# Performance work log

Hardware: AMD Instinct MI355X
Metric: run time of the kernel (lower is better)

## Reference

```python
import jax, jax.numpy as jnp
import numpy as np
from jax import lax

CONF_THR = 0.1
IOU_THR = 0.45
B, C, IMG = 4, 20, 416.0
SIZES = {"p3": 8112, "p4": 2028, "p5": 507}


def setup_inputs() -> dict:
    key = jax.random.key(0)
    ks = jax.random.split(key, 4 * len(SIZES))
    d = {}
    i = 0
    for name, n in SIZES.items():
        # valid xyxy boxes: random centers in image, widths/heights in [4, 104]
        cxy = jax.random.uniform(ks[i], (B, n, 2), jnp.float32) * IMG
        wh = jax.random.uniform(ks[i + 1], (B, n, 2), jnp.float32) * 100.0 + 4.0
        d[f"{name}_boxes"] = jnp.concatenate([cxy - wh / 2, cxy + wh / 2], axis=-1)
        d[f"{name}_conf"] = jax.random.uniform(ks[i + 2], (B, n, 1), jnp.float32)
        d[f"{name}_cls"] = jax.random.uniform(ks[i + 3], (B, n, C), jnp.float32)
        i += 4
    return d


def _iou_row(b, boxes, area_b, areas):
    # IoU of one box b [4] against all boxes [N,4] (same clamp math as torch _nms)
    xx1 = jnp.maximum(boxes[:, 0], b[0])
    yy1 = jnp.maximum(boxes[:, 1], b[1])
    xx2 = jnp.minimum(boxes[:, 2], b[2])
    yy2 = jnp.minimum(boxes[:, 3], b[3])
    inter = jnp.maximum(xx2 - xx1, 0.0) * jnp.maximum(yy2 - yy1, 0.0)
    return inter / (area_b + areas - inter)


def _nms_keep(boxes, scores, valid):
    # Greedy NMS on one image with padding. Returns (order, keep) so that
    # boxes[order][keep] matches torch's detections[keep-indices] set.
    n = boxes.shape[0]
    order = jnp.argsort(-scores)  # descending, as scores.sort(descending=True)
    sb = boxes[order]
    sv = valid[order]
    areas = (sb[:, 2] - sb[:, 0]) * (sb[:, 3] - sb[:, 1])
    idx = jnp.arange(n)

    def body(i, supp):
        keep_i = jnp.logical_and(sv[i], jnp.logical_not(supp[i]))
        iou = _iou_row(sb[i], sb, areas[i], areas)  # [N]
        return jnp.logical_or(supp, keep_i & (iou > IOU_THR) & (idx > i))

    supp = lax.fori_loop(0, n, body, jnp.zeros(n, bool))
    keep = jnp.logical_and(sv, jnp.logical_not(supp))
    return order, keep


def reference(p3_boxes, p3_conf, p3_cls, p4_boxes, p4_conf, p4_cls,
              p5_boxes, p5_conf, p5_cls):
    boxes = jnp.concatenate([p3_boxes, p4_boxes, p5_boxes], axis=1)   # [B,N,4]
    conf = jnp.concatenate([p3_conf, p4_conf, p5_conf], axis=1)[..., 0]  # [B,N]
    cls = jnp.concatenate([p3_cls, p4_cls, p5_cls], axis=1)           # [B,N,C]

    cls_conf = jnp.max(cls, axis=-1)
    cls_idx = jnp.argmax(cls, axis=-1)
    valid = conf > CONF_THR           # torch drops these; we mask (padded NMS)
    score = jnp.where(valid, conf * cls_conf, 0.0)

    order, keep = jax.vmap(_nms_keep)(boxes, score, valid)  # [B,N] each

    sb = jnp.take_along_axis(boxes, order[..., None], axis=1)
    ss = jnp.take_along_axis(score, order, axis=1)
    sc = jnp.take_along_axis(cls_idx, order, axis=1)
    out_score = jnp.where(keep, ss, 0.0)
    dets = jnp.concatenate(
        [sb, out_score[..., None], sc.astype(jnp.float32)[..., None]], axis=-1
    )  # [B,N,6] = (x1,y1,x2,y2,conf,class), score-sorted; keep marks survivors
    return dets, keep
```

## Files before the change

### kernel.cpp

```cpp
#include <hip/hip_runtime.h>
#include <stdint.h>

#define NB3 8112
#define NB4 2028
#define NB5 507
#define NTOT 10647
#define NBATCH 4
#define NCLS 20
#define NW32 333
#define NW64 167
#define NPAIR 84
#define NTAIL 23
#define RCH 11
#define RSL 6
#define RTP 7
#define LDS_CAP 9984
#define CONF_THR_F 0.1f
#define IOU_THR_F 0.45f
#define IOU_MID ((double)IOU_THR_F + 0x1p-26)

typedef unsigned long long u64;

__global__ void prep_kernel(const float* __restrict__ p3b, const float* __restrict__ p3c, const float* __restrict__ p3k,
                            const float* __restrict__ p4b, const float* __restrict__ p4c, const float* __restrict__ p4k,
                            const float* __restrict__ p5b, const float* __restrict__ p5c, const float* __restrict__ p5k,
                            uint64_t* __restrict__ keys, float4* __restrict__ boxes_cat,
                            float* __restrict__ score, int* __restrict__ clsidx, uint32_t* __restrict__ svout,
                            int* __restrict__ nvalid, int* __restrict__ rank)
{
#pragma clang fp contract(off)
    int idx = blockIdx.x * 256 + threadIdx.x;
    if (idx < NBATCH) nvalid[idx] = 0;
    if (idx >= NBATCH * NTOT) return;
    rank[idx] = 0;
    int b = idx / NTOT;
    int i = idx - b * NTOT;

    const float* bx; const float* cf; const float* cl; int n, off;
    if (i < NB3)            { bx = p3b; cf = p3c; cl = p3k; n = NB3; off = i; }
    else if (i < NB3 + NB4) { bx = p4b; cf = p4c; cl = p4k; n = NB4; off = i - NB3; }
    else                    { bx = p5b; cf = p5c; cl = p5k; n = NB5; off = i - NB3 - NB4; }

    size_t e = (size_t)b * n + off;
    float4 box = *(const float4*)(bx + e * 4);
    float conf = cf[e];
    const float* c = cl + e * NCLS;
    float m = c[0]; int mi = 0;
    #pragma unroll
    for (int k = 1; k < NCLS; ++k) { float v = c[k]; if (v > m) { m = v; mi = k; } }

    bool valid = conf > CONF_THR_F;
    float s = valid ? conf * m : 0.0f;
    uint32_t sb = __float_as_uint(s);
    keys[idx]      = ((uint64_t)sb << 32) | (uint32_t)(0xFFFFFFFFu - (uint32_t)i);
    boxes_cat[idx] = box;
    score[idx]     = s;
    clsidx[idx]    = mi;
    svout[idx]     = valid ? 1u : 0u;
}

__global__ void __launch_bounds__(256) rank_partial(const uint64_t* __restrict__ keys,
                                                    int* __restrict__ rank)
{
    int b = blockIdx.z;
    const uint64_t* kb = keys + (size_t)b * NTOT;
    int i0 = blockIdx.x * 1024 + threadIdx.x;
    uint64_t k0 = (i0       < NTOT) ? kb[i0]       : 0ull;
    uint64_t k1 = (i0 + 256 < NTOT) ? kb[i0 + 256] : 0ull;
    uint64_t k2 = (i0 + 512 < NTOT) ? kb[i0 + 512] : 0ull;
    uint64_t k3 = (i0 + 768 < NTOT) ? kb[i0 + 768] : 0ull;
    int r0 = 0, r1 = 0, r2 = 0, r3 = 0;

    __shared__ uint64_t tile[256];
    for (int tt = 0; tt < RTP; ++tt) {
        int j = (blockIdx.y * RTP + tt) * 256 + threadIdx.x;
        tile[threadIdx.x] = (j < NTOT) ? kb[j] : 0ull;
        __syncthreads();
        #pragma unroll 8
        for (int t = 0; t < 256; ++t) {
            uint64_t kt = tile[t];
            r0 += (kt > k0) ? 1 : 0;
            r1 += (kt > k1) ? 1 : 0;
            r2 += (kt > k2) ? 1 : 0;
            r3 += (kt > k3) ? 1 : 0;
        }
        __syncthreads();
    }

    int* rb = rank + (size_t)b * NTOT;
    if (i0       < NTOT) atomicAdd(&rb[i0],       r0);
    if (i0 + 256 < NTOT) atomicAdd(&rb[i0 + 256], r1);
    if (i0 + 512 < NTOT) atomicAdd(&rb[i0 + 512], r2);
    if (i0 + 768 < NTOT) atomicAdd(&rb[i0 + 768], r3);
}

__global__ void inv_kernel(const int* __restrict__ rank, int* __restrict__ inv)
{
    int idx = blockIdx.x * 256 + threadIdx.x;
    if (idx >= NBATCH * NTOT) return;
    int b = idx / NTOT;
    int i = idx - b * NTOT;
    inv[(size_t)b * NTOT + rank[idx]] = i;
}

__global__ void gather_kernel(const int* __restrict__ inv,
                              const float4* __restrict__ boxes_cat,
                              const float* __restrict__ score,
                              const int* __restrict__ clsidx,
                              const uint32_t* __restrict__ sv,
                              float4* __restrict__ sboxes, float* __restrict__ sscore,
                              int* __restrict__ scls, uint32_t* __restrict__ ssv,
                              int* __restrict__ nvalid, int need_nvalid)
{
    int idx = blockIdx.x * 256 + threadIdx.x;
    if (idx >= NBATCH * NTOT) return;
    int b = idx / NTOT;
    int i = idx - b * NTOT;
    size_t base = (size_t)b * NTOT;
    int src = inv[idx];
    float4 box = boxes_cat[base + src];
    uint32_t v = sv[base + src];
    sboxes[idx] = box;
    sscore[idx] = score[base + src];
    scls[idx]   = clsidx[base + src];
    ssv[idx]    = v;
    if (need_nvalid) {
        int mv = v ? (i + 1) : 0;
        #pragma unroll
        for (int d = 32; d >= 1; d >>= 1) {
            int o = __shfl_xor(mv, d, 64);
            mv = (o > mv) ? o : mv;
        }
        if ((threadIdx.x & 63) == 0 && mv > 0) atomicMax(&nvalid[b], mv);
    }
}

__global__ void __launch_bounds__(256) mask_build(const float4* __restrict__ sboxes,
                                                  u64* __restrict__ mask,
                                                  u64* __restrict__ ldiag,
                                                  u64* __restrict__ s1diag,
                                                  u64* __restrict__ s2diag,
                                                  u64* __restrict__ s3diag,
                                                  u64* __restrict__ s4diag,
                                                  u64* __restrict__ s5diag)
{
#pragma clang fp contract(off)
    int c = blockIdx.y;
    if (c < blockIdx.x * 4) return;
    int b = blockIdx.z;
    int sub = threadIdx.x >> 6;
    int lane = threadIdx.x & 63;
    int r = blockIdx.x * 4 + sub;

    __shared__ float4 cb[64];
    __shared__ float  ca[64];
    if (threadIdx.x < 64) {
        int j = c * 64 + threadIdx.x;
        float4 bj = sboxes[(size_t)b * NTOT + (j < NTOT ? j : NTOT - 1)];
        cb[threadIdx.x] = bj;
        ca[threadIdx.x] = (bj.z - bj.x) * (bj.w - bj.y);
    }
    __syncthreads();

    if (r >= NW64 || c < r) return;
    int i = r * 64 + lane;
    float4 bi = sboxes[(size_t)b * NTOT + (i < NTOT ? i : NTOT - 1)];
    float ax1 = bi.x, ay1 = bi.y, ax2 = bi.z, ay2 = bi.w;
    float area_i = (ax2 - ax1) * (ay2 - ay1);

    u64 hh = 0;
    #pragma unroll 8
    for (int k = 0; k < 64; ++k) {
        float4 bj = cb[k];
        float xx1 = fmaxf(bj.x, ax1);
        float yy1 = fmaxf(bj.y, ay1);
        float xx2 = fminf(bj.z, ax2);
        float yy2 = fminf(bj.w, ay2);
        float w = fmaxf(xx2 - xx1, 0.0f);
        float h = fmaxf(yy2 - yy1, 0.0f);
        float inter = w * h;
        float uni = (area_i + ca[k]) - inter;
        bool hit = (double)inter > IOU_MID * (double)uni;
        hh |= (u64)hit << k;
    }

    if (i < NTOT) {
        u64 colmask = (c == NW64 - 1) ? ((1ull << NTAIL) - 1) : ~0ull;
        u64 mw = hh & colmask;
        size_t bl = ((size_t)b * NW64 + r) * 64 + lane;
        if (c == r) {
            u64 gtmask = (lane < 63) ? (~0ull << (lane + 1)) : 0ull;
            mask[((size_t)b * NTOT + i) * NW64 + c] = mw & gtmask;
            ldiag[bl] = hh & ((1ull << lane) - 1);
        } else {
            mask[((size_t)b * NTOT + i) * NW64 + c] = mw;
            if (c == r + 1) s1diag[bl] = mw;
            if (c == r + 2) s2diag[bl] = mw;
            if (c == r + 3) s3diag[bl] = mw;
            if (c == r + 4) s4diag[bl] = mw;
            if (c == r + 5) s5diag[bl] = mw;
        }
    }
}

static __device__ __forceinline__ void bar_sync()
{
    asm volatile("s_waitcnt lgkmcnt(0)" ::: "memory");
    __builtin_amdgcn_s_barrier();
    asm volatile("" ::: "memory");
}

static __device__ __forceinline__ u64 rfl64(u64 x)
{
    uint32_t lo = __builtin_amdgcn_readfirstlane((uint32_t)x);
    uint32_t hi = __builtin_amdgcn_readfirstlane((uint32_t)(x >> 32));
    return ((u64)hi << 32) | (u64)lo;
}

__global__ void __launch_bounds__(1024) resolve_kernel(const u64* __restrict__ mask,
                                                       const u64* __restrict__ ldiag,
                                                       const u64* __restrict__ s1diag,
                                                       const u64* __restrict__ s2diag,
                                                       const u64* __restrict__ s3diag,
                                                       const u64* __restrict__ s4diag,
                                                       const u64* __restrict__ s5diag,
                                                       const float4* __restrict__ sboxes,
                                                       const float* __restrict__ sscore,
                                                       const int* __restrict__ scls,
                                                       const uint32_t* __restrict__ ssv,
                                                       u64* __restrict__ rem_out,
                                                       float* __restrict__ out)
{
    int b = blockIdx.x;
    int tid = threadIdx.x;
    int lane = tid & 63;
    int wv = tid >> 6;
    const u64* M  = mask   + (size_t)b * NTOT * NW64;
    const u64* LD = ldiag  + (size_t)b * NW64 * 64;
    const u64* S1A = s1diag + (size_t)b * NW64 * 64;
    const u64* S2A = s2diag + (size_t)b * NW64 * 64;
    const u64* S3A = s3diag + (size_t)b * NW64 * 64;
    const u64* S4A = s4diag + (size_t)b * NW64 * 64;
    const u64* S5A = s5diag + (size_t)b * NW64 * 64;

    __shared__ u64 rem_s[NW64 + 1];
    __shared__ u64 v_s[NW64 + 1];
    __shared__ u64 kept_s[2][2];
    __shared__ int klist[2][128];
    __shared__ u64 sc_s;

    for (int t = tid; t < NW64 + 1; t += 1024) rem_s[t] = 0ull;
    for (int t = wv; t < NW64; t += 16) {
        int i = t * 64 + lane;
        uint32_t v = (i < NTOT) ? ssv[(size_t)b * NTOT + i] : 0u;
        u64 w = __ballot(v != 0u);
        if (lane == 0) v_s[t] = w;
    }
    if (tid == 0) {
        v_s[NW64] = 0ull;
        kept_s[0][0] = kept_s[0][1] = kept_s[1][0] = kept_s[1][1] = 0ull;
        klist[0][0] = 0; klist[1][0] = 0; sc_s = 0ull;
    }

    u64 ld0 = 0, s1_0 = 0, s2_0 = 0, s3_0 = 0, s4_0 = 0, s5_0 = 0;
    u64 ld1 = 0, s1_1 = 0, s2_1 = 0, s3_1 = 0, s4_1 = 0;
    if (wv == 0) {
        ld0 = LD[lane];
        s1_0 = S1A[lane]; s2_0 = S2A[lane]; s3_0 = S3A[lane];
        s4_0 = S4A[lane]; s5_0 = S5A[lane];
        ld1 = LD[64 + lane];
        s1_1 = S1A[64 + lane]; s2_1 = S2A[64 + lane];
        s3_1 = S3A[64 + lane]; s4_1 = S4A[64 + lane];
    }

    u64 df[5][3];
    #pragma unroll
    for (int t = 0; t < 5; ++t) {
        #pragma unroll
        for (int c = 0; c < 3; ++c) df[t][c] = 0ull;
    }

    bar_sync();

    for (int p = 0; p < NPAIR; ++p) {
        int par = p & 1;
        int w0 = 2 * p, w1 = 2 * p + 1;

        if (wv == 0) {
            u64 a0pre = rfl64(v_s[w0] & ~rem_s[w0]);
            u64 a1pre = rfl64(v_s[w1] & ~rem_s[w1]);

            u64 U = a0pre, K0 = 0;
            while (U) {
                u64 UK = U | K0;
                bool inU = (U >> lane) & 1;
                u64 nk = __ballot(inU && ((ld0 & UK) == 0ull));
                u64 nr = __ballot(inU && ((ld0 & K0) != 0ull));
                K0 |= nk;
                U &= ~(nk | nr);
            }

            if (lane == 0) sc_s = 0ull;
            if (((K0 >> lane) & 1) && s1_0)
                atomicOr((unsigned long long*)&sc_s, (unsigned long long)s1_0);
            asm volatile("s_waitcnt lgkmcnt(0)" ::: "memory");
            u64 S1 = sc_s;

            u64 U1 = a1pre & ~S1, K1 = 0;
            while (U1) {
                u64 UK = U1 | K1;
                bool inU = (U1 >> lane) & 1;
                u64 nk = __ballot(inU && ((ld1 & UK) == 0ull));
                u64 nr = __ballot(inU && ((ld1 & K1) != 0ull));
                K1 |= nk;
                U1 &= ~(nk | nr);
            }

            if (lane == 0) {
                kept_s[par][0] = K0; kept_s[par][1] = K1;
                u64 sup0 = a0pre & ~K0;
                u64 sup1 = a1pre & ~K1;
                if (sup0) rem_s[w0] |= sup0;
                if (sup1) rem_s[w1] |= sup1;
            }
            int w2 = w0 + 2, w3 = w0 + 3, w4 = w0 + 4, w5 = w0 + 5;
            bool h2 = w2 < NW64, h3 = w3 < NW64, h4 = w4 < NW64, h5 = w5 < NW64;
            if ((K0 >> lane) & 1) {
                if (h2 && s2_0) atomicOr((unsigned long long*)&rem_s[w2], (unsigned long long)s2_0);
                if (h3 && s3_0) atomicOr((unsigned long long*)&rem_s[w3], (unsigned long long)s3_0);
                if (h4 && s4_0) atomicOr((unsigned long long*)&rem_s[w4], (unsigned long long)s4_0);
                if (h5 && s5_0) atomicOr((unsigned long long*)&rem_s[w5], (unsigned long long)s5_0);
            }
            if ((K1 >> lane) & 1) {
                if (h2 && s1_1) atomicOr((unsigned long long*)&rem_s[w2], (unsigned long long)s1_1);
                if (h3 && s2_1) atomicOr((unsigned long long*)&rem_s[w3], (unsigned long long)s2_1);
                if (h4 && s3_1) atomicOr((unsigned long long*)&rem_s[w4], (unsigned long long)s3_1);
                if (h5 && s4_1) atomicOr((unsigned long long*)&rem_s[w5], (unsigned long long)s4_1);
            }
            int pn = (p + 1 < NPAIR) ? p + 1 : p;
            int i0 = 2 * pn;
            int i1 = (2 * pn + 1 < NW64) ? 2 * pn + 1 : NW64 - 1;
            ld0  = LD [(size_t)i0 * 64 + lane];
            s1_0 = S1A[(size_t)i0 * 64 + lane];
            s2_0 = S2A[(size_t)i0 * 64 + lane];
            s3_0 = S3A[(size_t)i0 * 64 + lane];
            s4_0 = S4A[(size_t)i0 * 64 + lane];
            s5_0 = S5A[(size_t)i0 * 64 + lane];
            ld1  = LD [(size_t)i1 * 64 + lane];
            s1_1 = S1A[(size_t)i1 * 64 + lane];
            s2_1 = S2A[(size_t)i1 * 64 + lane];
            s3_1 = S3A[(size_t)i1 * 64 + lane];
            s4_1 = S4A[(size_t)i1 * 64 + lane];
        } else {
            int parw = par ^ 1;
            u64 k0 = kept_s[parw][0], k1 = kept_s[parw][1];
            int n0 = __popcll(k0);
            int nk = n0 + __popcll(k1);
            u64 below = (1ull << lane) - 1;
            if ((k0 >> lane) & 1) klist[parw][__popcll(k0 & below)] = lane;
            if ((k1 >> lane) & 1) klist[parw][n0 + __popcll(k1 & below)] = 64 + lane;

            #pragma unroll
            for (int t = 0; t < 5; ++t) {
                #pragma unroll
                for (int c = 0; c < 3; ++c) {
                    if (df[t][c])
                        atomicOr((unsigned long long*)&rem_s[2 * p + 2 + (c << 6) + lane],
                                 (unsigned long long)df[t][c]);
                }
            }

            int q = (p > 0) ? p - 1 : 0;
            int nkc = (nk < 64) ? nk : 64;
            #pragma unroll
            for (int t = 0; t < 5; ++t) {
                int s = (wv - 1) + t * 15;
                bool has = (p > 0) && (s < nkc);
                int rr = klist[parw][has ? s : 0];
                const u64* R = M + (size_t)(q * 128 + rr) * NW64;
                #pragma unroll
                for (int c = 0; c < 3; ++c) {
                    int w = 2 * q + 6 + (c << 6) + lane;
                    df[t][c] = (has && w < NW64) ? R[w] : 0ull;
                }
            }
            for (int base = 64; base < nk; base += 64) {
                #pragma unroll
                for (int t = 0; t < 5; ++t) {
                    int s = base + (wv - 1) + t * 15;
                    bool has = s < nk;
                    int rr = klist[parw][has ? s : 0];
                    const u64* R = M + (size_t)(q * 128 + rr) * NW64;
                    #pragma unroll
                    for (int c = 0; c < 3; ++c) {
                        int w = 2 * q + 6 + (c << 6) + lane;
                        u64 v2 = (has && w < NW64) ? R[w] : 0ull;
                        if (v2) atomicOr((unsigned long long*)&rem_s[w], (unsigned long long)v2);
                    }
                }
            }
        }

        bar_sync();
    }


    for (int t = tid; t < NW64; t += 1024)
        rem_out[(size_t)b * NW64 + t] = rem_s[t];

    for (int t = tid; t < NTOT; t += 1024) {
        size_t idx = (size_t)b * NTOT + t;
        float4 box = sboxes[idx];
        u64 rw = rem_s[t >> 6];
        bool keep = (ssv[idx] != 0u) && !((rw >> (t & 63)) & 1ull);
        float sc = keep ? sscore[idx] : 0.0f;
        float* d = out + idx * 6;
        d[0] = box.x; d[1] = box.y; d[2] = box.z; d[3] = box.w;
        d[4] = sc;    d[5] = (float)scls[idx];
        out[(size_t)NBATCH * NTOT * 6 + idx] = keep ? 1.0f : 0.0f;
    }
}

extern __shared__ unsigned char nms_smem[];

__global__ void __launch_bounds__(1024) nms_kernel(const float4* __restrict__ sboxes,
                                                   const uint32_t* __restrict__ ssv,
                                                   const int* __restrict__ nvalid_arr,
                                                   uint32_t* __restrict__ supp_out)
{
#pragma clang fp contract(off)
    int b = blockIdx.x;
    float4*   lbox = (float4*)nms_smem;
    uint32_t* supp = (uint32_t*)(nms_smem + (size_t)LDS_CAP * 16);
    uint32_t* svb  = supp + NW32;

    int nv = nvalid_arr[b];
    const float4* gb = sboxes + (size_t)b * NTOT;
    const uint32_t* gv = ssv + (size_t)b * NTOT;

    for (int t = threadIdx.x; t < NW32; t += 1024) { supp[t] = 0u; svb[t] = 0u; }
    __syncthreads();
    for (int t = threadIdx.x; t < nv; t += 1024) {
        if (t < LDS_CAP) lbox[t] = gb[t];
        if (gv[t]) atomicOr(&svb[t >> 5], 1u << (t & 31));
    }
    __syncthreads();

    for (int i = 0; i < nv; ++i) {
        uint32_t sw = supp[i >> 5];
        if ((sw >> (i & 31)) & 1u) continue;
        uint32_t vw = svb[i >> 5];
        if (!((vw >> (i & 31)) & 1u)) continue;

        float4 bi = (i < LDS_CAP) ? lbox[i] : gb[i];
        float ax1 = bi.x, ay1 = bi.y, ax2 = bi.z, ay2 = bi.w;
        float area_i = (ax2 - ax1) * (ay2 - ay1);

        for (int j = i + 1 + (int)threadIdx.x; j < nv; j += 1024) {
            float4 bj = (j < LDS_CAP) ? lbox[j] : gb[j];
            float xx1 = fmaxf(bj.x, ax1);
            float yy1 = fmaxf(bj.y, ay1);
            float xx2 = fminf(bj.z, ax2);
            float yy2 = fminf(bj.w, ay2);
            float w = fmaxf(xx2 - xx1, 0.0f);
            float h = fmaxf(yy2 - yy1, 0.0f);
            float inter  = w * h;
            float area_j = (bj.z - bj.x) * (bj.w - bj.y);
            float iou = inter / ((area_i + area_j) - inter);
            if (iou > IOU_THR_F) atomicOr(&supp[j >> 5], 1u << (j & 31));
        }
        __syncthreads();
    }

    __syncthreads();
    for (int t = threadIdx.x; t < NW32; t += 1024)
        supp_out[(size_t)b * (2 * NW64) + t] = supp[t];
}

__global__ void out_kernel(const float4* __restrict__ sboxes, const float* __restrict__ sscore,
                           const int* __restrict__ scls, const uint32_t* __restrict__ ssv,
                           const u64* __restrict__ rem, float* __restrict__ out)
{
    int idx = blockIdx.x * 256 + threadIdx.x;
    if (idx >= NBATCH * NTOT) return;
    int b = idx / NTOT;
    int p = idx - b * NTOT;

    float4 box = sboxes[idx];
    u64 rw = rem[(size_t)b * NW64 + (p >> 6)];
    bool keep = (ssv[idx] != 0u) && !((rw >> (p & 63)) & 1ull);
    float sc = keep ? sscore[idx] : 0.0f;

    float* d = out + (size_t)idx * 6;
    d[0] = box.x; d[1] = box.y; d[2] = box.z; d[3] = box.w;
    d[4] = sc;    d[5] = (float)scls[idx];
    out[(size_t)NBATCH * NTOT * 6 + idx] = keep ? 1.0f : 0.0f;
}

extern "C" void kernel_launch(void* const* d_in, const int* in_sizes, int n_in,
                              void* d_out, int out_size, void* d_ws, size_t ws_size,
                              hipStream_t stream)
{
    const float* p3b = (const float*)d_in[0];
    const float* p3c = (const float*)d_in[1];
    const float* p3k = (const float*)d_in[2];
    const float* p4b = (const float*)d_in[3];
    const float* p4c = (const float*)d_in[4];
    const float* p4k = (const float*)d_in[5];
    const float* p5b = (const float*)d_in[6];
    const float* p5c = (const float*)d_in[7];
    const float* p5k = (const float*)d_in[8];
    float* out = (float*)d_out;

    char* ws = (char*)d_ws;
    size_t off = 0;
    auto alloc = [&](size_t bytes) { size_t o = off; off += (bytes + 255) & ~(size_t)255; return o; };
    const size_t BN = (size_t)NBATCH * NTOT;
    uint64_t* keys      = (uint64_t*)(ws + alloc(BN * 8));
    float4*   boxes_cat = (float4*)  (ws + alloc(BN * 16));
    float*    score     = (float*)   (ws + alloc(BN * 4));
    int*      clsidx    = (int*)     (ws + alloc(BN * 4));
    uint32_t* sv        = (uint32_t*)(ws + alloc(BN * 4));
    int*      rank_arr  = (int*)     (ws + alloc(BN * 4));
    int*      inv_arr   = (int*)     (ws + alloc(BN * 4));
    float4*   sboxes    = (float4*)  (ws + alloc(BN * 16));
    float*    sscore    = (float*)   (ws + alloc(BN * 4));
    int*      scls      = (int*)     (ws + alloc(BN * 4));
    uint32_t* ssv       = (uint32_t*)(ws + alloc(BN * 4));
    u64*      rem64     = (u64*)     (ws + alloc((size_t)NBATCH * NW64 * 8));
    int*      nvalid    = (int*)     (ws + alloc(NBATCH * 4));
    u64*      ldiag     = (u64*)     (ws + alloc((size_t)NBATCH * NW64 * 64 * 8));
    u64*      s1diag    = (u64*)     (ws + alloc((size_t)NBATCH * NW64 * 64 * 8));
    u64*      s2diag    = (u64*)     (ws + alloc((size_t)NBATCH * NW64 * 64 * 8));
    u64*      s3diag    = (u64*)     (ws + alloc((size_t)NBATCH * NW64 * 64 * 8));
    u64*      s4diag    = (u64*)     (ws + alloc((size_t)NBATCH * NW64 * 64 * 8));
    u64*      s5diag    = (u64*)     (ws + alloc((size_t)NBATCH * NW64 * 64 * 8));
    u64*      mask      = (u64*)     (ws + alloc((size_t)NBATCH * NTOT * NW64 * 8));
    bool fast = (off <= ws_size);

    int nblk = (int)((BN + 255) / 256);
    prep_kernel<<<nblk, 256, 0, stream>>>(p3b, p3c, p3k, p4b, p4c, p4k, p5b, p5c, p5k,
                                          keys, boxes_cat, score, clsidx, sv,
                                          nvalid, rank_arr);

    dim3 rpgrid(RCH, RSL, NBATCH);
    rank_partial<<<rpgrid, 256, 0, stream>>>(keys, rank_arr);

    inv_kernel<<<nblk, 256, 0, stream>>>(rank_arr, inv_arr);

    gather_kernel<<<nblk, 256, 0, stream>>>(inv_arr, boxes_cat, score, clsidx, sv,
                                            sboxes, sscore, scls, ssv,
                                            nvalid, fast ? 0 : 1);

    if (fast) {
        dim3 mgrid((NW64 + 3) / 4, NW64, NBATCH);
        mask_build<<<mgrid, 256, 0, stream>>>(sboxes, mask, ldiag, s1diag, s2diag,
                                              s3diag, s4diag, s5diag);
        resolve_kernel<<<NBATCH, 1024, 0, stream>>>(mask, ldiag, s1diag, s2diag, s3diag,
                                                    s4diag, s5diag,
                                                    sboxes, sscore, scls, ssv,
                                                    rem64, out);
    } else {
        hipMemsetAsync(rem64, 0, (size_t)NBATCH * NW64 * 8, stream);
        size_t smem = (size_t)LDS_CAP * 16 + (size_t)NW32 * 4 * 2;
        smem = (smem + 15) & ~(size_t)15;
        hipFuncSetAttribute((const void*)nms_kernel, hipFuncAttributeMaxDynamicSharedMemorySize, (int)smem);
        nms_kernel<<<NBATCH, 1024, smem, stream>>>(sboxes, ssv, nvalid, (uint32_t*)rem64);
        out_kernel<<<nblk, 256, 0, stream>>>(sboxes, sscore, scls, ssv, rem64, out);
    }
}
```

Baseline: 432.0 us.

## Resolve both words of a pair jointly using transposed cross-word mask and prefetch

mask_build now writes a transposed copy of the first super-diagonal block for each even row word (lt1), giving each column box its suppressors from the previous word. resolve_kernel uses it to run the greedy fixed-point iteration over both 64-box words at once, removing the serial LDS atomic round trip and the second while loop. The next pair's diagonal loads are also issued before the iteration instead of after, so their latency overlaps the compute. The cost is extra ballots in mask_build for those blocks, more live registers in wave 0, and a new global buffer.

```diff
diff --git a/kernel.cpp b/kernel.cpp
--- a/kernel.cpp
+++ b/kernel.cpp
@@ -142,7 +142,8 @@
                                                   u64* __restrict__ s2diag,
                                                   u64* __restrict__ s3diag,
                                                   u64* __restrict__ s4diag,
-                                                  u64* __restrict__ s5diag)
+                                                  u64* __restrict__ s5diag,
+                                                  u64* __restrict__ lt1)
 {
 #pragma clang fp contract(off)
     int c = blockIdx.y;
@@ -184,9 +185,10 @@
         hh |= (u64)hit << k;
     }
 
+    u64 colmask = (c == NW64 - 1) ? ((1ull << NTAIL) - 1) : ~0ull;
+    u64 mw = hh & colmask;
+
     if (i < NTOT) {
-        u64 colmask = (c == NW64 - 1) ? ((1ull << NTAIL) - 1) : ~0ull;
-        u64 mw = hh & colmask;
         size_t bl = ((size_t)b * NW64 + r) * 64 + lane;
         if (c == r) {
             u64 gtmask = (lane < 63) ? (~0ull << (lane + 1)) : 0ull;
@@ -201,6 +203,15 @@
             if (c == r + 5) s5diag[bl] = mw;
         }
     }
+    if (c == r + 1 && (r & 1) == 0) {
+        u64 ltw = 0;
+        #pragma unroll 8
+        for (int k = 0; k < 64; ++k) {
+            u64 bw = __ballot((mw >> k) & 1ull);
+            if (lane == k) ltw = bw;
+        }
+        lt1[((size_t)b * NPAIR + (r >> 1)) * 64 + lane] = ltw;
+    }
 }
 
 static __device__ __forceinline__ void bar_sync()
@@ -224,6 +235,7 @@
                                                        const u64* __restrict__ s3diag,
                                                        const u64* __restrict__ s4diag,
                                                        const u64* __restrict__ s5diag,
+                                                       const u64* __restrict__ lt1,
                                                        const float4* __restrict__ sboxes,
                                                        const float* __restrict__ sscore,
                                                        const int* __restrict__ scls,
@@ -235,19 +247,19 @@
     int tid = threadIdx.x;
     int lane = tid & 63;
     int wv = tid >> 6;
-    const u64* M  = mask   + (size_t)b * NTOT * NW64;
-    const u64* LD = ldiag  + (size_t)b * NW64 * 64;
+    const u64* M   = mask   + (size_t)b * NTOT * NW64;
+    const u64* LD  = ldiag  + (size_t)b * NW64 * 64;
     const u64* S1A = s1diag + (size_t)b * NW64 * 64;
     const u64* S2A = s2diag + (size_t)b * NW64 * 64;
     const u64* S3A = s3diag + (size_t)b * NW64 * 64;
     const u64* S4A = s4diag + (size_t)b * NW64 * 64;
     const u64* S5A = s5diag + (size_t)b * NW64 * 64;
+    const u64* LT  = lt1    + (size_t)b * NPAIR * 64;
 
     __shared__ u64 rem_s[NW64 + 1];
     __shared__ u64 v_s[NW64 + 1];
     __shared__ u64 kept_s[2][2];
     __shared__ int klist[2][128];
-    __shared__ u64 sc_s;
 
     for (int t = tid; t < NW64 + 1; t += 1024) rem_s[t] = 0ull;
     for (int t = wv; t < NW64; t += 16) {
@@ -259,16 +271,16 @@
     if (tid == 0) {
         v_s[NW64] = 0ull;
         kept_s[0][0] = kept_s[0][1] = kept_s[1][0] = kept_s[1][1] = 0ull;
-        klist[0][0] = 0; klist[1][0] = 0; sc_s = 0ull;
-    }
-
-    u64 ld0 = 0, s1_0 = 0, s2_0 = 0, s3_0 = 0, s4_0 = 0, s5_0 = 0;
-    u64 ld1 = 0, s1_1 = 0, s2_1 = 0, s3_1 = 0, s4_1 = 0;
+        klist[0][0] = 0; klist[1][0] = 0;
+    }
+
+    u64 ld0 = 0, ld1 = 0, lt = 0;
+    u64 s1_0 = 0, s2_0 = 0, s3_0 = 0, s4_0 = 0, s5_0 = 0;
+    u64 s1_1 = 0, s2_1 = 0, s3_1 = 0, s4_1 = 0;
     if (wv == 0) {
-        ld0 = LD[lane];
+        ld0 = LD[lane];      ld1 = LD[64 + lane];   lt = LT[lane];
         s1_0 = S1A[lane]; s2_0 = S2A[lane]; s3_0 = S3A[lane];
         s4_0 = S4A[lane]; s5_0 = S5A[lane];
-        ld1 = LD[64 + lane];
         s1_1 = S1A[64 + lane]; s2_1 = S2A[64 + lane];
         s3_1 = S3A[64 + lane]; s4_1 = S4A[64 + lane];
     }
@@ -287,39 +299,41 @@
         int w0 = 2 * p, w1 = 2 * p + 1;
 
         if (wv == 0) {
-            u64 a0pre = rfl64(v_s[w0] & ~rem_s[w0]);
-            u64 a1pre = rfl64(v_s[w1] & ~rem_s[w1]);
-
-            u64 U = a0pre, K0 = 0;
-            while (U) {
-                u64 UK = U | K0;
-                bool inU = (U >> lane) & 1;
-                u64 nk = __ballot(inU && ((ld0 & UK) == 0ull));
-                u64 nr = __ballot(inU && ((ld0 & K0) != 0ull));
-                K0 |= nk;
-                U &= ~(nk | nr);
-            }
-
-            if (lane == 0) sc_s = 0ull;
-            if (((K0 >> lane) & 1) && s1_0)
-                atomicOr((unsigned long long*)&sc_s, (unsigned long long)s1_0);
-            asm volatile("s_waitcnt lgkmcnt(0)" ::: "memory");
-            u64 S1 = sc_s;
-
-            u64 U1 = a1pre & ~S1, K1 = 0;
-            while (U1) {
-                u64 UK = U1 | K1;
-                bool inU = (U1 >> lane) & 1;
-                u64 nk = __ballot(inU && ((ld1 & UK) == 0ull));
-                u64 nr = __ballot(inU && ((ld1 & K1) != 0ull));
-                K1 |= nk;
-                U1 &= ~(nk | nr);
+            int pn = (p + 1 < NPAIR) ? p + 1 : p;
+            int i0 = 2 * pn;
+            int i1 = (2 * pn + 1 < NW64) ? 2 * pn + 1 : NW64 - 1;
+            u64 nld0 = LD [(size_t)i0 * 64 + lane];
+            u64 nld1 = LD [(size_t)i1 * 64 + lane];
+            u64 nlt  = LT [(size_t)pn * 64 + lane];
+            u64 ns1_0 = S1A[(size_t)i0 * 64 + lane];
+            u64 ns2_0 = S2A[(size_t)i0 * 64 + lane];
+            u64 ns3_0 = S3A[(size_t)i0 * 64 + lane];
+            u64 ns4_0 = S4A[(size_t)i0 * 64 + lane];
+            u64 ns5_0 = S5A[(size_t)i0 * 64 + lane];
+            u64 ns1_1 = S1A[(size_t)i1 * 64 + lane];
+            u64 ns2_1 = S2A[(size_t)i1 * 64 + lane];
+            u64 ns3_1 = S3A[(size_t)i1 * 64 + lane];
+            u64 ns4_1 = S4A[(size_t)i1 * 64 + lane];
+
+            u64 a0 = rfl64(v_s[w0] & ~rem_s[w0]);
+            u64 a1 = rfl64(v_s[w1] & ~rem_s[w1]);
+            u64 U0 = a0, U1 = a1, K0 = 0, K1 = 0;
+            while (U0 | U1) {
+                u64 UK0 = U0 | K0, UK1 = U1 | K1;
+                bool in0 = (U0 >> lane) & 1;
+                bool in1 = (U1 >> lane) & 1;
+                u64 nk0 = __ballot(in0 && (ld0 & UK0) == 0ull);
+                u64 nk1 = __ballot(in1 && ((lt & UK0) | (ld1 & UK1)) == 0ull);
+                u64 nr0 = __ballot(in0 && (ld0 & K0) != 0ull);
+                u64 nr1 = __ballot(in1 && ((lt & K0) | (ld1 & K1)) != 0ull);
+                K0 |= nk0; K1 |= nk1;
+                U0 &= ~(nk0 | nr0); U1 &= ~(nk1 | nr1);
             }
 
             if (lane == 0) {
                 kept_s[par][0] = K0; kept_s[par][1] = K1;
-                u64 sup0 = a0pre & ~K0;
-                u64 sup1 = a1pre & ~K1;
+                u64 sup0 = a0 & ~K0;
+                u64 sup1 = a1 & ~K1;
                 if (sup0) rem_s[w0] |= sup0;
                 if (sup1) rem_s[w1] |= sup1;
             }
@@ -337,20 +351,9 @@
                 if (h4 && s3_1) atomicOr((unsigned long long*)&rem_s[w4], (unsigned long long)s3_1);
                 if (h5 && s4_1) atomicOr((unsigned long long*)&rem_s[w5], (unsigned long long)s4_1);
             }
-            int pn = (p + 1 < NPAIR) ? p + 1 : p;
-            int i0 = 2 * pn;
-            int i1 = (2 * pn + 1 < NW64) ? 2 * pn + 1 : NW64 - 1;
-            ld0  = LD [(size_t)i0 * 64 + lane];
-            s1_0 = S1A[(size_t)i0 * 64 + lane];
-            s2_0 = S2A[(size_t)i0 * 64 + lane];
-            s3_0 = S3A[(size_t)i0 * 64 + lane];
-            s4_0 = S4A[(size_t)i0 * 64 + lane];
-            s5_0 = S5A[(size_t)i0 * 64 + lane];
-            ld1  = LD [(size_t)i1 * 64 + lane];
-            s1_1 = S1A[(size_t)i1 * 64 + lane];
-            s2_1 = S2A[(size_t)i1 * 64 + lane];
-            s3_1 = S3A[(size_t)i1 * 64 + lane];
-            s4_1 = S4A[(size_t)i1 * 64 + lane];
+            ld0 = nld0; ld1 = nld1; lt = nlt;
+            s1_0 = ns1_0; s2_0 = ns2_0; s3_0 = ns3_0; s4_0 = ns4_0; s5_0 = ns5_0;
+            s1_1 = ns1_1; s2_1 = ns2_1; s3_1 = ns3_1; s4_1 = ns4_1;
         } else {
             int parw = par ^ 1;
             u64 k0 = kept_s[parw][0], k1 = kept_s[parw][1];
@@ -535,6 +538,7 @@
     u64*      s3diag    = (u64*)     (ws + alloc((size_t)NBATCH * NW64 * 64 * 8));
     u64*      s4diag    = (u64*)     (ws + alloc((size_t)NBATCH * NW64 * 64 * 8));
     u64*      s5diag    = (u64*)     (ws + alloc((size_t)NBATCH * NW64 * 64 * 8));
+    u64*      lt1       = (u64*)     (ws + alloc((size_t)NBATCH * NPAIR * 64 * 8));
     u64*      mask      = (u64*)     (ws + alloc((size_t)NBATCH * NTOT * NW64 * 8));
     bool fast = (off <= ws_size);
 
@@ -555,9 +559,9 @@
     if (fast) {
         dim3 mgrid((NW64 + 3) / 4, NW64, NBATCH);
         mask_build<<<mgrid, 256, 0, stream>>>(sboxes, mask, ldiag, s1diag, s2diag,
-                                              s3diag, s4diag, s5diag);
+                                              s3diag, s4diag, s5diag, lt1);
         resolve_kernel<<<NBATCH, 1024, 0, stream>>>(mask, ldiag, s1diag, s2diag, s3diag,
-                                                    s4diag, s5diag,
+                                                    s4diag, s5diag, lt1,
                                                     sboxes, sscore, scls, ssv,
                                                     rem64, out);
     } else {
```

Result: no change. 432.0 us (-0.0%).
